# Kernel optimization log

Measured on AMD Instinct MI355X. Metric: run time of the kernel, lower is better.

## Reference

```python
import jax, jax.numpy as jnp
import numpy as np

# ---- quantization constants (8-bit, per-tensor affine; representative values) ----
Q_MAX = 255.0
S_IN, Z_IN = 0.05, 128.0      # block input
S1, Z1 = 0.04, 128.0          # after expand 1x1 + hardswish
S2, Z2 = 0.04, 128.0          # after depthwise 5x5 + hardswish
S_SE1, Z_SE1 = 0.03, 128.0    # SE fc1 output
S_SE2, Z_SE2 = 1.0 / 255.0, 0.0  # SE fc2 hardsigmoid output in [0,1]
S_MUL, Z_MUL = 0.04, 128.0    # SE gated activation
S3, Z3 = 0.05, 128.0          # after project 1x1
S_OUT, Z_OUT = 0.06, 128.0    # after residual add
W_SCALE = 0.01                # symmetric per-tensor weight scale (zero_point = 0)
EXP_C = 576                   # expanded channels (depthwise groups)


def conv(x, w, stride=1, padding=0, groups=1):
    return jax.lax.conv_general_dilated(
        x, w, (stride, stride), [(padding, padding), (padding, padding)],
        feature_group_count=groups, dimension_numbers=('NCHW', 'OIHW', 'NCHW'))


def hardswish(x):
    return x * jnp.clip(x + 3.0, 0.0, 6.0) * (1.0 / 6.0)


def hardsigmoid(x):
    return jnp.clip(x + 3.0, 0.0, 6.0) * (1.0 / 6.0)


def qconv(x_q, w_q, b_q, s_in, z_in, s_out, z_out, stride=1, padding=0, groups=1, act=None):
    """Quantized conv: int-domain accumulation (simulated in fp32), fused activation
    on the dequantized accumulator, then requantize to [0, Q_MAX]."""
    acc = conv(x_q - z_in, w_q, stride, padding, groups) + b_q[None, :, None, None]
    deq = acc * (s_in * W_SCALE)  # dequantize accumulator
    if act == 'hardswish':
        deq = hardswish(deq)
    elif act == 'hardsigmoid':
        deq = hardsigmoid(deq)
    return jnp.clip(deq * (1.0 / s_out) + z_out, 0.0, Q_MAX)


def setup_inputs() -> dict:
    key = jax.random.key(0)
    ks = jax.random.split(key, 11)
    def qw(k, shape):  # int8-style symmetric weights stored as fp32 integers
        return jnp.round(jnp.clip(jax.random.normal(k, shape) * 40.0, -127.0, 127.0))
    def qb(k, n):      # int32-style bias in accumulator domain
        return jnp.round(jax.random.normal(k, (n,)) * 500.0)
    return {
        'x':      jnp.round(jax.random.uniform(ks[0], (64, 96, 28, 28)) * Q_MAX),
        'w_exp':  qw(ks[1], (576, 96, 1, 1)),  'b_exp':  qb(ks[2], 576),
        'w_dw':   qw(ks[3], (576, 1, 5, 5)),   'b_dw':   qb(ks[4], 576),
        'w_se1':  qw(ks[5], (144, 576, 1, 1)), 'b_se1':  qb(ks[6], 144),
        'w_se2':  qw(ks[7], (576, 144, 1, 1)), 'b_se2':  qb(ks[8], 576),
        'w_proj': qw(ks[9], (96, 576, 1, 1)),  'b_proj': qb(ks[10], 96),
    }


def reference(x, w_exp, b_exp, w_dw, b_dw, w_se1, b_se1, w_se2, b_se2, w_proj, b_proj):
    # expand 1x1 (+ hardswish)
    e = qconv(x, w_exp, b_exp, S_IN, Z_IN, S1, Z1, act='hardswish')
    # depthwise 5x5, padding=(5-1)//2=2, groups=expanded (+ hardswish)
    d = qconv(e, w_dw, b_dw, S1, Z1, S2, Z2, padding=2, groups=EXP_C, act='hardswish')
    # squeeze-excitation: global avg pool -> fc1 -> fc2(hardsigmoid) -> quantized mul
    pooled = jnp.mean(d, axis=(2, 3), keepdims=True)  # [N, 576, 1, 1]
    g1 = qconv(pooled, w_se1, b_se1, S2, Z2, S_SE1, Z_SE1)
    g2 = qconv(g1, w_se2, b_se2, S_SE1, Z_SE1, S_SE2, Z_SE2, act='hardsigmoid')
    gated = jnp.clip((g2 - Z_SE2) * (d - Z2) * (S_SE2 * S2 / S_MUL) + Z_MUL, 0.0, Q_MAX)
    # project 1x1 (linear)
    p = qconv(gated, w_proj, b_proj, S_MUL, Z_MUL, S3, Z3)
    # quantized residual add (stride=1, in==out channels -> use_res_connect)
    out = jnp.clip((x - Z_IN) * (S_IN / S_OUT) + (p - Z3) * (S3 / S_OUT) + Z_OUT, 0.0, Q_MAX)
    return out
```

## Files before the change

### kernel.cpp

```cpp
#include <hip/hip_runtime.h>

typedef _Float16 v8h __attribute__((ext_vector_type(8)));
typedef _Float16 v4h __attribute__((ext_vector_type(4)));
typedef _Float16 v2h __attribute__((ext_vector_type(2)));
typedef float v4f __attribute__((ext_vector_type(4)));

#define NB 64
#define CI 96
#define CE 576
#define CO 96
#define HW 784
#define SEC 144

#if defined(__has_builtin)
#if __has_builtin(__builtin_amdgcn_fdot2)
#define HAVE_FDOT2 1
#endif
#endif

__device__ __forceinline__ float fdot2(v2h a, v2h b, float c) {
#ifdef HAVE_FDOT2
  return __builtin_amdgcn_fdot2(a, b, c, false);
#else
  return (float)a[0] * (float)b[0] + ((float)a[1] * (float)b[1] + c);
#endif
}

__global__ __launch_bounds__(256) void k0_cvt_w(const float* __restrict__ w_exp,
                                                const float* __restrict__ w_proj,
                                                _Float16* __restrict__ w_exp_h,
                                                _Float16* __restrict__ w_proj_h) {
  int i = blockIdx.x * 256 + threadIdx.x;
  if (i < CE * CI) {
    w_exp_h[i]  = (_Float16)w_exp[i];
    w_proj_h[i] = (_Float16)w_proj[i];
  }
}

__global__ __launch_bounds__(384) void k1_expand(const float* __restrict__ x,
                                                 const _Float16* __restrict__ w_exp_h,
                                                 const float* __restrict__ b_exp,
                                                 _Float16* __restrict__ e_s) {
  __shared__ _Float16 x_lds[112][104];
  const int tid = threadIdx.x;
  const int n   = blockIdx.z;
  const int co0 = blockIdx.y * 96;
  const int hw0 = blockIdx.x * 112;

  for (int idx = tid; idx < CI * 28; idx += 384) {
    int c = idx / 28, seg = idx % 28;
    const float4 v = *(const float4*)&x[(n * CI + c) * HW + hw0 + seg * 4];
    int row = seg * 4;
    x_lds[row + 0][c] = (_Float16)(v.x - 128.0f);
    x_lds[row + 1][c] = (_Float16)(v.y - 128.0f);
    x_lds[row + 2][c] = (_Float16)(v.z - 128.0f);
    x_lds[row + 3][c] = (_Float16)(v.w - 128.0f);
  }
  __syncthreads();

  const int wv = tid >> 6, lane = tid & 63;
  const int l15 = lane & 15, q = lane >> 4;

  const _Float16* wrow = &w_exp_h[(co0 + wv * 16 + l15) * CI + q * 8];
  v8h a0 = *(const v8h*)(wrow);
  v8h a1 = *(const v8h*)(wrow + 32);
  v8h a2 = *(const v8h*)(wrow + 64);

  v4f acc[7];
#pragma unroll
  for (int t = 0; t < 7; ++t) acc[t] = (v4f){0.f, 0.f, 0.f, 0.f};

#pragma unroll
  for (int t = 0; t < 7; ++t) {
    const _Float16* bp = &x_lds[t * 16 + l15][q * 8];
    v8h b0 = *(const v8h*)(bp);
    v8h b1 = *(const v8h*)(bp + 32);
    v8h b2 = *(const v8h*)(bp + 64);
    acc[t] = __builtin_amdgcn_mfma_f32_16x16x32_f16(a0, b0, acc[t], 0, 0, 0);
    acc[t] = __builtin_amdgcn_mfma_f32_16x16x32_f16(a1, b1, acc[t], 0, 0, 0);
    acc[t] = __builtin_amdgcn_mfma_f32_16x16x32_f16(a2, b2, acc[t], 0, 0, 0);
  }

  float bia[4];
#pragma unroll
  for (int r = 0; r < 4; ++r) bia[r] = b_exp[co0 + wv * 16 + q * 4 + r];

#pragma unroll
  for (int t = 0; t < 7; ++t) {
#pragma unroll
    for (int r = 0; r < 4; ++r) {
      int co = co0 + wv * 16 + q * 4 + r;
      int hw = hw0 + t * 16 + l15;
      float deq = (acc[t][r] + bia[r]) * 5.0e-4f;
      float cl  = fminf(fmaxf(deq + 3.0f, 0.0f), 6.0f);
      float hs  = deq * cl * (1.0f / 6.0f);
      float ev  = fminf(fmaxf(hs * 25.0f, -128.0f), 127.0f);
      e_s[(n * CE + co) * HW + hw] = (_Float16)ev;
    }
  }
}

__global__ __launch_bounds__(256, 4) void k2_dw(const _Float16* __restrict__ e_s,
                                                const float* __restrict__ w_dw,
                                                const float* __restrict__ b_dw,
                                                _Float16* __restrict__ d_s,
                                                float* __restrict__ d_sums) {
  __shared__ _Float16 e_lds[8][32][36];
  __shared__ _Float16 w_pairs[8][5][8];
  const int tid = threadIdx.x;
  const int n = blockIdx.y;
  const int c0 = blockIdx.x * 8;

  {
    unsigned long long* z = (unsigned long long*)&e_lds[0][0][0];
    for (int idx = tid; idx < 8 * 32 * 36 * 2 / 8; idx += 256) z[idx] = 0ull;
  }
  for (int idx = tid; idx < 320; idx += 256) {
    int c = idx / 40, r = idx % 40, dy = r / 8, k = r % 8;
    int tap = (k < 4) ? k : (k - 3);
    w_pairs[c][dy][k] = (_Float16)w_dw[(c0 + c) * 25 + dy * 5 + tap];
  }
  __syncthreads();
  for (int idx = tid; idx < 1568; idx += 256) {
    int c = idx / 196, r = idx % 196, y = r / 7, j = r % 7;
    v4h v = *(const v4h*)&e_s[(n * CE + c0 + c) * HW + y * 28 + j * 4];
    *(v4h*)&e_lds[c][2 + y][4 + j * 4] = v;
  }
  __syncthreads();

  const int c = tid >> 5, l = tid & 31;
  v2h W01[5], W23[5], W12[5], W34[5];
  float W0s[5], W4s[5];
#pragma unroll
  for (int dy = 0; dy < 5; ++dy) {
    W01[dy] = *(const v2h*)&w_pairs[c][dy][0];
    W23[dy] = *(const v2h*)&w_pairs[c][dy][2];
    W12[dy] = *(const v2h*)&w_pairs[c][dy][4];
    W34[dy] = *(const v2h*)&w_pairs[c][dy][6];
    W0s[dy] = (float)W01[dy][0];
    W4s[dy] = (float)W34[dy][1];
  }
  const float bc = b_dw[c0 + c];

  float csum = 0.0f;
  if (l < 28) {
    const int y = l;
    v2h P0[5], P1[5], P2[5], P3[5];
#pragma unroll
    for (int dy = 0; dy < 5; ++dy) {
      const _Float16* row = &e_lds[c][y + dy][0];
      P0[dy] = *(const v2h*)(row + 2);
      P1[dy] = *(const v2h*)(row + 4);
      P2[dy] = *(const v2h*)(row + 6);
      P3[dy] = *(const v2h*)(row + 8);
    }
#pragma unroll
    for (int x0 = 0; x0 < 28; x0 += 4) {
      float o0 = bc, o1 = bc, o2 = bc, o3 = bc;
#pragma unroll
      for (int dy = 0; dy < 5; ++dy) {
        o0 = fdot2(P0[dy], W01[dy], o0);
        o0 = fdot2(P1[dy], W23[dy], o0);
        o0 += (float)P2[dy][0] * W4s[dy];
        o1 += (float)P0[dy][1] * W0s[dy];
        o1 = fdot2(P1[dy], W12[dy], o1);
        o1 = fdot2(P2[dy], W34[dy], o1);
        o2 = fdot2(P1[dy], W01[dy], o2);
        o2 = fdot2(P2[dy], W23[dy], o2);
        o2 += (float)P3[dy][0] * W4s[dy];
        o3 += (float)P1[dy][1] * W0s[dy];
        o3 = fdot2(P2[dy], W12[dy], o3);
        o3 = fdot2(P3[dy], W34[dy], o3);
      }
      v4h dv;
      float oo[4] = {o0, o1, o2, o3};
#pragma unroll
      for (int i = 0; i < 4; ++i) {
        float deq = oo[i] * 4.0e-4f;
        float cl  = fminf(fmaxf(deq + 3.0f, 0.0f), 6.0f);
        float hs  = deq * cl * (1.0f / 6.0f);
        float dvv = fminf(fmaxf(hs * 25.0f, -128.0f), 127.0f);
        dv[i] = (_Float16)dvv;
        csum += dvv;
      }
      *(v4h*)&d_s[(n * CE + c0 + c) * HW + y * 28 + x0] = dv;
      if (x0 < 24) {
#pragma unroll
        for (int dy = 0; dy < 5; ++dy) {
          const _Float16* row = &e_lds[c][y + dy][0];
          P0[dy] = P2[dy];
          P1[dy] = P3[dy];
          P2[dy] = *(const v2h*)(row + x0 + 10);
          P3[dy] = *(const v2h*)(row + x0 + 12);
        }
      }
    }
  }
#pragma unroll
  for (int m = 16; m >= 1; m >>= 1) csum += __shfl_xor(csum, m);
  if (l == 0) d_sums[n * CE + c0 + c] = csum;
}

__global__ __launch_bounds__(256) void k3a_fc1(const float* __restrict__ d_sums,
                                               const float* __restrict__ w_se1,
                                               const float* __restrict__ b_se1,
                                               float* __restrict__ g1) {
  const int tid = threadIdx.x;
  const int wv = tid >> 6, lane = tid & 63;
  const int n = blockIdx.y;
  const int o = blockIdx.x * 4 + wv;
  const float* wrow = &w_se1[o * CE];
  const float* srow = &d_sums[n * CE];
  float p = 0.f;
#pragma unroll
  for (int s = 0; s < 9; ++s) {
    int cc = lane + s * 64;
    p += wrow[cc] * srow[cc];
  }
#pragma unroll
  for (int m = 32; m >= 1; m >>= 1) p += __shfl_xor(p, m);
  if (lane == 0) {
    float deq = (p * (1.0f / 784.0f) + b_se1[o]) * 4.0e-4f;
    g1[n * SEC + o] = fminf(fmaxf(deq * 33.3333333f + 128.0f, 0.0f), 255.0f) - 128.0f;
  }
}

__global__ __launch_bounds__(256) void k3b_fc2(const float* __restrict__ g1,
                                               const float* __restrict__ w_se2,
                                               const float* __restrict__ b_se2,
                                               float* __restrict__ g2p) {
  const int tid = threadIdx.x;
  const int wv = tid >> 6, lane = tid & 63;
  const int n = blockIdx.y;
  const int o = blockIdx.x * 4 + wv;
  const float* wrow = &w_se2[o * SEC];
  const float* grow = &g1[n * SEC];
  float p = wrow[lane] * grow[lane] + wrow[lane + 64] * grow[lane + 64];
  if (lane < 16) p += wrow[lane + 128] * grow[lane + 128];
#pragma unroll
  for (int m = 32; m >= 1; m >>= 1) p += __shfl_xor(p, m);
  if (lane == 0) {
    float deq = (p + b_se2[o]) * 3.0e-4f;
    g2p[n * CE + o] = fminf(fmaxf(deq + 3.0f, 0.0f), 6.0f) * (1.0f / 6.0f);
  }
}

__global__ __launch_bounds__(384) void k4_proj(const _Float16* __restrict__ d_s,
                                               const float* __restrict__ g2p,
                                               const _Float16* __restrict__ w_proj_h,
                                               const float* __restrict__ b_proj,
                                               const float* __restrict__ x,
                                               float* __restrict__ out) {
  __shared__ _Float16 B_lds[112][40];
  __shared__ float g2l[CE];
  const int tid = threadIdx.x;
  const int n = blockIdx.y;
  const int hw0 = blockIdx.x * 112;

  for (int i = tid; i < CE; i += 384) g2l[i] = g2p[n * CE + i];
  __syncthreads();

  const int wv = tid >> 6, lane = tid & 63;
  const int l15 = lane & 15, q = lane >> 4;

  v4f acc[7];
#pragma unroll
  for (int t = 0; t < 7; ++t) acc[t] = (v4f){0.f, 0.f, 0.f, 0.f};

  for (int ks = 0; ks < 18; ++ks) {
    for (int idx = tid; idx < 896; idx += 384) {
      int cg = idx / 28, seg = idx % 28;
      int cc = ks * 32 + cg;
      v4h dv = *(const v4h*)&d_s[(n * CE + cc) * HW + hw0 + seg * 4];
      float g = g2l[cc];
      int r0 = seg * 4;
      B_lds[r0 + 0][cg] = (_Float16)(g * (float)dv[0]);
      B_lds[r0 + 1][cg] = (_Float16)(g * (float)dv[1]);
      B_lds[r0 + 2][cg] = (_Float16)(g * (float)dv[2]);
      B_lds[r0 + 3][cg] = (_Float16)(g * (float)dv[3]);
    }
    __syncthreads();
    v8h a = *(const v8h*)&w_proj_h[(wv * 16 + l15) * CE + ks * 32 + q * 8];
#pragma unroll
    for (int t = 0; t < 7; ++t) {
      v8h b = *(const v8h*)&B_lds[t * 16 + l15][q * 8];
      acc[t] = __builtin_amdgcn_mfma_f32_16x16x32_f16(a, b, acc[t], 0, 0, 0);
    }
    __syncthreads();
  }

  float bia[4];
#pragma unroll
  for (int r = 0; r < 4; ++r) bia[r] = b_proj[wv * 16 + q * 4 + r];

#pragma unroll
  for (int t = 0; t < 7; ++t) {
#pragma unroll
    for (int r = 0; r < 4; ++r) {
      int co = wv * 16 + q * 4 + r;
      int hw = hw0 + t * 16 + l15;
      float p = fminf(fmaxf((acc[t][r] + bia[r]) * 4.0e-4f * 20.0f + 128.0f, 0.0f), 255.0f);
      float xv = x[(n * CO + co) * HW + hw];
      float o = (xv - 128.0f) * 0.8333333333f + (p - 128.0f) * 0.8333333333f + 128.0f;
      out[(n * CO + co) * HW + hw] = fminf(fmaxf(o, 0.0f), 255.0f);
    }
  }
}

extern "C" void kernel_launch(void* const* d_in, const int* in_sizes, int n_in,
                              void* d_out, int out_size, void* d_ws, size_t ws_size,
                              hipStream_t stream) {
  const float* x      = (const float*)d_in[0];
  const float* w_exp  = (const float*)d_in[1];
  const float* b_exp  = (const float*)d_in[2];
  const float* w_dw   = (const float*)d_in[3];
  const float* b_dw   = (const float*)d_in[4];
  const float* w_se1  = (const float*)d_in[5];
  const float* b_se1  = (const float*)d_in[6];
  const float* w_se2  = (const float*)d_in[7];
  const float* b_se2  = (const float*)d_in[8];
  const float* w_proj = (const float*)d_in[9];
  const float* b_proj = (const float*)d_in[10];
  float* out = (float*)d_out;

  char* ws = (char*)d_ws;
  const size_t SZ_W  = (size_t)CE * CI * 2;
  const size_t SZ_ED = (size_t)NB * CE * HW * 2;
  const size_t SZ_S  = (size_t)NB * CE * 4;
  _Float16* w_exp_h  = (_Float16*)(ws);
  _Float16* w_proj_h = (_Float16*)(ws + SZ_W);
  _Float16* e_s      = (_Float16*)(ws + 2 * SZ_W);
  _Float16* d_s      = (_Float16*)(ws + 2 * SZ_W + SZ_ED);
  float*    d_sums   = (float*)   (ws + 2 * SZ_W + 2 * SZ_ED);
  float*    g2p      = (float*)   (ws + 2 * SZ_W + 2 * SZ_ED + SZ_S);
  float*    g1       = (float*)   (ws + 2 * SZ_W + 2 * SZ_ED + 2 * SZ_S);

  k0_cvt_w<<<(CE * CI + 255) / 256, 256, 0, stream>>>(w_exp, w_proj, w_exp_h, w_proj_h);
  k1_expand<<<dim3(7, 6, NB), 384, 0, stream>>>(x, w_exp_h, b_exp, e_s);
  k2_dw<<<dim3(72, NB), 256, 0, stream>>>(e_s, w_dw, b_dw, d_s, d_sums);
  k3a_fc1<<<dim3(36, NB), 256, 0, stream>>>(d_sums, w_se1, b_se1, g1);
  k3b_fc2<<<dim3(144, NB), 256, 0, stream>>>(g1, w_se2, b_se2, g2p);
  k4_proj<<<dim3(7, NB), 384, 0, stream>>>(d_s, g2p, w_proj_h, b_proj, x, out);
}
```

Before: 207.1 us.

## Store depthwise output channel-blocked and feed projection MFMA directly from global

```diff
diff --git a/kernel.cpp b/kernel.cpp
--- a/kernel.cpp
+++ b/kernel.cpp
@@ -41,20 +41,24 @@
                                                  const _Float16* __restrict__ w_exp_h,
                                                  const float* __restrict__ b_exp,
                                                  _Float16* __restrict__ e_s) {
-  __shared__ _Float16 x_lds[112][104];
+  __shared__ _Float16 xf[3 * 7 * 520];
   const int tid = threadIdx.x;
   const int n   = blockIdx.z;
   const int co0 = blockIdx.y * 96;
   const int hw0 = blockIdx.x * 112;
 
-  for (int idx = tid; idx < CI * 28; idx += 384) {
+#pragma unroll
+  for (int it = 0; it < 7; ++it) {
+    int idx = it * 384 + tid;
     int c = idx / 28, seg = idx % 28;
     const float4 v = *(const float4*)&x[(n * CI + c) * HW + hw0 + seg * 4];
-    int row = seg * 4;
-    x_lds[row + 0][c] = (_Float16)(v.x - 128.0f);
-    x_lds[row + 1][c] = (_Float16)(v.y - 128.0f);
-    x_lds[row + 2][c] = (_Float16)(v.z - 128.0f);
-    x_lds[row + 3][c] = (_Float16)(v.w - 128.0f);
+    int s = c >> 5, q = (c >> 3) & 3, j = c & 7;
+    int t = seg >> 2, l0 = (seg & 3) * 4;
+    int base = (s * 7 + t) * 520 + (q * 16 + l0) * 8 + j;
+    xf[base]      = (_Float16)(v.x - 128.0f);
+    xf[base + 8]  = (_Float16)(v.y - 128.0f);
+    xf[base + 16] = (_Float16)(v.z - 128.0f);
+    xf[base + 24] = (_Float16)(v.w - 128.0f);
   }
   __syncthreads();
 
@@ -72,10 +76,9 @@
 
 #pragma unroll
   for (int t = 0; t < 7; ++t) {
-    const _Float16* bp = &x_lds[t * 16 + l15][q * 8];
-    v8h b0 = *(const v8h*)(bp);
-    v8h b1 = *(const v8h*)(bp + 32);
-    v8h b2 = *(const v8h*)(bp + 64);
+    v8h b0 = *(const v8h*)&xf[(0 * 7 + t) * 520 + lane * 8];
+    v8h b1 = *(const v8h*)&xf[(1 * 7 + t) * 520 + lane * 8];
+    v8h b2 = *(const v8h*)&xf[(2 * 7 + t) * 520 + lane * 8];
     acc[t] = __builtin_amdgcn_mfma_f32_16x16x32_f16(a0, b0, acc[t], 0, 0, 0);
     acc[t] = __builtin_amdgcn_mfma_f32_16x16x32_f16(a1, b1, acc[t], 0, 0, 0);
     acc[t] = __builtin_amdgcn_mfma_f32_16x16x32_f16(a2, b2, acc[t], 0, 0, 0);
@@ -103,10 +106,11 @@
 __global__ __launch_bounds__(256, 4) void k2_dw(const _Float16* __restrict__ e_s,
                                                 const float* __restrict__ w_dw,
                                                 const float* __restrict__ b_dw,
-                                                _Float16* __restrict__ d_s,
+                                                _Float16* __restrict__ d_t,
                                                 float* __restrict__ d_sums) {
   __shared__ _Float16 e_lds[8][32][36];
   __shared__ _Float16 w_pairs[8][5][8];
+  __shared__ _Float16 d_tile[784 * 9];
   const int tid = threadIdx.x;
   const int n = blockIdx.y;
   const int c0 = blockIdx.x * 8;
@@ -172,7 +176,6 @@
         o3 = fdot2(P2[dy], W12[dy], o3);
         o3 = fdot2(P3[dy], W34[dy], o3);
       }
-      v4h dv;
       float oo[4] = {o0, o1, o2, o3};
 #pragma unroll
       for (int i = 0; i < 4; ++i) {
@@ -180,10 +183,9 @@
         float cl  = fminf(fmaxf(deq + 3.0f, 0.0f), 6.0f);
         float hs  = deq * cl * (1.0f / 6.0f);
         float dvv = fminf(fmaxf(hs * 25.0f, -128.0f), 127.0f);
-        dv[i] = (_Float16)dvv;
+        d_tile[(y * 28 + x0 + i) * 9 + c] = (_Float16)dvv;
         csum += dvv;
       }
-      *(v4h*)&d_s[(n * CE + c0 + c) * HW + y * 28 + x0] = dv;
       if (x0 < 24) {
 #pragma unroll
         for (int dy = 0; dy < 5; ++dy) {
@@ -199,6 +201,15 @@
 #pragma unroll
   for (int m = 16; m >= 1; m >>= 1) csum += __shfl_xor(csum, m);
   if (l == 0) d_sums[n * CE + c0 + c] = csum;
+
+  __syncthreads();
+  const size_t obase = ((size_t)n * 72 + (c0 >> 3)) * 784;
+  for (int hw = tid; hw < 784; hw += 256) {
+    v8h o;
+#pragma unroll
+    for (int j = 0; j < 8; ++j) o[j] = d_tile[hw * 9 + j];
+    *(v8h*)&d_t[(obase + hw) * 8] = o;
+  }
 }
 
 __global__ __launch_bounds__(256) void k3a_fc1(const float* __restrict__ d_sums,
@@ -228,7 +239,7 @@
 __global__ __launch_bounds__(256) void k3b_fc2(const float* __restrict__ g1,
                                                const float* __restrict__ w_se2,
                                                const float* __restrict__ b_se2,
-                                               float* __restrict__ g2p) {
+                                               _Float16* __restrict__ g2h) {
   const int tid = threadIdx.x;
   const int wv = tid >> 6, lane = tid & 63;
   const int n = blockIdx.y;
@@ -241,69 +252,45 @@
   for (int m = 32; m >= 1; m >>= 1) p += __shfl_xor(p, m);
   if (lane == 0) {
     float deq = (p + b_se2[o]) * 3.0e-4f;
-    g2p[n * CE + o] = fminf(fmaxf(deq + 3.0f, 0.0f), 6.0f) * (1.0f / 6.0f);
-  }
-}
-
-__global__ __launch_bounds__(384) void k4_proj(const _Float16* __restrict__ d_s,
-                                               const float* __restrict__ g2p,
+    g2h[n * CE + o] =
+        (_Float16)(fminf(fmaxf(deq + 3.0f, 0.0f), 6.0f) * (1.0f / 6.0f));
+  }
+}
+
+__global__ __launch_bounds__(384) void k4_proj(const _Float16* __restrict__ d_t,
+                                               const _Float16* __restrict__ g2h,
                                                const _Float16* __restrict__ w_proj_h,
                                                const float* __restrict__ b_proj,
                                                const float* __restrict__ x,
                                                float* __restrict__ out) {
-  __shared__ _Float16 B_lds[112][40];
-  __shared__ float g2l[CE];
   const int tid = threadIdx.x;
   const int n = blockIdx.y;
-  const int hw0 = blockIdx.x * 112;
-
-  for (int i = tid; i < CE; i += 384) g2l[i] = g2p[n * CE + i];
-  __syncthreads();
-
+  const int hw0 = blockIdx.x * 16;
   const int wv = tid >> 6, lane = tid & 63;
   const int l15 = lane & 15, q = lane >> 4;
 
-  v4f acc[7];
-#pragma unroll
-  for (int t = 0; t < 7; ++t) acc[t] = (v4f){0.f, 0.f, 0.f, 0.f};
-
+  v4f acc = (v4f){0.f, 0.f, 0.f, 0.f};
+  const _Float16* dbase = d_t + (((size_t)n * 72 + q) * 784 + hw0 + l15) * 8;
+  const _Float16* abase = &w_proj_h[(wv * 16 + l15) * CE + q * 8];
+  const _Float16* gbase = &g2h[(size_t)n * CE + q * 8];
+
+#pragma unroll 3
   for (int ks = 0; ks < 18; ++ks) {
-    for (int idx = tid; idx < 896; idx += 384) {
-      int cg = idx / 28, seg = idx % 28;
-      int cc = ks * 32 + cg;
-      v4h dv = *(const v4h*)&d_s[(n * CE + cc) * HW + hw0 + seg * 4];
-      float g = g2l[cc];
-      int r0 = seg * 4;
-      B_lds[r0 + 0][cg] = (_Float16)(g * (float)dv[0]);
-      B_lds[r0 + 1][cg] = (_Float16)(g * (float)dv[1]);
-      B_lds[r0 + 2][cg] = (_Float16)(g * (float)dv[2]);
-      B_lds[r0 + 3][cg] = (_Float16)(g * (float)dv[3]);
-    }
-    __syncthreads();
-    v8h a = *(const v8h*)&w_proj_h[(wv * 16 + l15) * CE + ks * 32 + q * 8];
-#pragma unroll
-    for (int t = 0; t < 7; ++t) {
-      v8h b = *(const v8h*)&B_lds[t * 16 + l15][q * 8];
-      acc[t] = __builtin_amdgcn_mfma_f32_16x16x32_f16(a, b, acc[t], 0, 0, 0);
-    }
-    __syncthreads();
-  }
-
-  float bia[4];
-#pragma unroll
-  for (int r = 0; r < 4; ++r) bia[r] = b_proj[wv * 16 + q * 4 + r];
-
-#pragma unroll
-  for (int t = 0; t < 7; ++t) {
-#pragma unroll
-    for (int r = 0; r < 4; ++r) {
-      int co = wv * 16 + q * 4 + r;
-      int hw = hw0 + t * 16 + l15;
-      float p = fminf(fmaxf((acc[t][r] + bia[r]) * 4.0e-4f * 20.0f + 128.0f, 0.0f), 255.0f);
-      float xv = x[(n * CO + co) * HW + hw];
-      float o = (xv - 128.0f) * 0.8333333333f + (p - 128.0f) * 0.8333333333f + 128.0f;
-      out[(n * CO + co) * HW + hw] = fminf(fmaxf(o, 0.0f), 255.0f);
-    }
+    v8h b = *(const v8h*)(dbase + (size_t)ks * (4 * 784 * 8));
+    v8h a = *(const v8h*)(abase + ks * 32);
+    v8h g = *(const v8h*)(gbase + ks * 32);
+    b = b * g;
+    acc = __builtin_amdgcn_mfma_f32_16x16x32_f16(a, b, acc, 0, 0, 0);
+  }
+
+#pragma unroll
+  for (int r = 0; r < 4; ++r) {
+    int co = wv * 16 + q * 4 + r;
+    int hw = hw0 + l15;
+    float p = fminf(fmaxf((acc[r] + b_proj[co]) * 4.0e-4f * 20.0f + 128.0f, 0.0f), 255.0f);
+    float xv = x[(n * CO + co) * HW + hw];
+    float o = (xv - 128.0f) * 0.8333333333f + (p - 128.0f) * 0.8333333333f + 128.0f;
+    out[(n * CO + co) * HW + hw] = fminf(fmaxf(o, 0.0f), 255.0f);
   }
 }
 
@@ -330,15 +317,15 @@
   _Float16* w_exp_h  = (_Float16*)(ws);
   _Float16* w_proj_h = (_Float16*)(ws + SZ_W);
   _Float16* e_s      = (_Float16*)(ws + 2 * SZ_W);
-  _Float16* d_s      = (_Float16*)(ws + 2 * SZ_W + SZ_ED);
+  _Float16* d_t      = (_Float16*)(ws + 2 * SZ_W + SZ_ED);
   float*    d_sums   = (float*)   (ws + 2 * SZ_W + 2 * SZ_ED);
-  float*    g2p      = (float*)   (ws + 2 * SZ_W + 2 * SZ_ED + SZ_S);
-  float*    g1       = (float*)   (ws + 2 * SZ_W + 2 * SZ_ED + 2 * SZ_S);
+  float*    g1       = (float*)   (ws + 2 * SZ_W + 2 * SZ_ED + SZ_S);
+  _Float16* g2h      = (_Float16*)(ws + 2 * SZ_W + 2 * SZ_ED + 2 * SZ_S);
 
   k0_cvt_w<<<(CE * CI + 255) / 256, 256, 0, stream>>>(w_exp, w_proj, w_exp_h, w_proj_h);
   k1_expand<<<dim3(7, 6, NB), 384, 0, stream>>>(x, w_exp_h, b_exp, e_s);
-  k2_dw<<<dim3(72, NB), 256, 0, stream>>>(e_s, w_dw, b_dw, d_s, d_sums);
+  k2_dw<<<dim3(72, NB), 256, 0, stream>>>(e_s, w_dw, b_dw, d_t, d_sums);
   k3a_fc1<<<dim3(36, NB), 256, 0, stream>>>(d_sums, w_se1, b_se1, g1);
-  k3b_fc2<<<dim3(144, NB), 256, 0, stream>>>(g1, w_se2, b_se2, g2p);
-  k4_proj<<<dim3(7, NB), 384, 0, stream>>>(d_s, g2p, w_proj_h, b_proj, x, out);
-}
+  k3b_fc2<<<dim3(144, NB), 256, 0, stream>>>(g1, w_se2, b_se2, g2h);
+  k4_proj<<<dim3(49, NB), 384, 0, stream>>>(d_t, g2h, w_proj_h, b_proj, x, out);
+}
```

Measured after the change: 229.7 us. 1.11x slower.
